# Kernel optimization log

Measured on AMD Instinct MI355X. Metric: run time of the kernel, lower is better.

The kernel has to match this reference:

```python
import jax, jax.numpy as jnp
import numpy as np

VOCAB = 50257
D_MEAN = 1024
D_MV = 1024
BATCH = 32
SEQ_LEN = 128


def setup_inputs() -> dict:
    key = jax.random.key(0)
    k_z, k_lab, k_w0, k_w1 = jax.random.split(key, 4)
    z = jax.random.normal(k_z, (BATCH, D_MEAN), dtype=jnp.float32)
    labels = jax.random.randint(k_lab, (BATCH, SEQ_LEN), 0, VOCAB, dtype=jnp.int64)
    # Linear weights stored as [in, out]; scaled like kaiming-uniform-ish init
    W0 = jax.random.normal(k_w0, (D_MEAN, D_MV), dtype=jnp.float32) * (1.0 / np.sqrt(D_MEAN))
    b0 = jnp.zeros((D_MV,), dtype=jnp.float32)
    W1 = jax.random.normal(k_w1, (D_MV, VOCAB), dtype=jnp.float32) * (1.0 / np.sqrt(D_MV))
    b1 = jnp.zeros((VOCAB,), dtype=jnp.float32)
    return {"z": z, "labels": labels, "W0": W0, "b0": b0, "W1": W1, "b1": b1}


def reference(z, labels, W0, b0, W1, b1):
    # bow_head: Linear -> Dropout(eval=identity) -> GELU -> Linear -> Dropout
    h = jax.nn.gelu(z @ W0 + b0, approximate=False)        # [B, d_mean_var]
    logits = h @ W1 + b1                                   # [B, vocab]
    # CrossEntropyLoss over logits expanded across seq_len == mean over
    # (B*seq_len) of NLL; log_softmax computed once per batch row and the
    # label gather reused across seq_len (same math, no expand materialized).
    logp = jax.nn.log_softmax(logits, axis=-1)             # [B, vocab]
    nll = -jnp.take_along_axis(logp, labels, axis=1)       # [B, seq_len]
    return jnp.mean(nll)
```

## Files before the change

### kernel.cpp

```cpp
#include <hip/hip_runtime.h>
#include <math.h>

#define VOCAB 50257
#define DMEAN 1024
#define DMV   1024
#define BATCH 32
#define SEQLEN 128
#define NS1 32
#define NS2 8
#define KC2 (DMV / NS2)
#define VP  50304
#define VPH (VP / 2)
#define CH3 2048
#define NB3 ((VP + CH3 - 1) / CH3)

static __device__ inline unsigned f2bf(float x) {
    unsigned u = __float_as_uint(x);
    return (u + 0x7fffu + ((u >> 16) & 1u)) >> 16;
}

__global__ __launch_bounds__(256) void k1_partial(const float* __restrict__ z,
                                                  const float* __restrict__ W0,
                                                  float* __restrict__ part) {
    int tx = threadIdx.x;
    int j  = blockIdx.x * 256 + tx;
    int k0 = blockIdx.y * (DMEAN / NS1);
    float acc[BATCH];
#pragma unroll
    for (int r = 0; r < BATCH; ++r) acc[r] = 0.f;
#pragma unroll 8
    for (int k = k0; k < k0 + (DMEAN / NS1); ++k) {
        float w = W0[k * DMV + j];
#pragma unroll
        for (int r = 0; r < BATCH; ++r)
            acc[r] = fmaf(z[r * DMEAN + k], w, acc[r]);
    }
#pragma unroll
    for (int r = 0; r < BATCH; ++r)
        part[(blockIdx.y * BATCH + r) * DMV + j] = acc[r];
}

__global__ __launch_bounds__(256) void k1_combine(const float* __restrict__ part,
                                                  const float* __restrict__ b0,
                                                  float* __restrict__ hT) {
    int t  = blockIdx.x * 256 + threadIdx.x;
    int e0 = t * 4;
    int r  = e0 >> 10;
    int j  = e0 & 1023;
    float4 s = *(const float4*)(b0 + j);
#pragma unroll
    for (int kb = 0; kb < NS1; ++kb) {
        float4 p = *(const float4*)(part + kb * BATCH * DMV + e0);
        s.x += p.x; s.y += p.y; s.z += p.z; s.w += p.w;
    }
    float v[4] = {s.x, s.y, s.z, s.w};
#pragma unroll
    for (int u = 0; u < 4; ++u) {
        float g = 0.5f * v[u] * (1.f + erff(v[u] * 0.70710678118654752f));
        hT[(j + u) * BATCH + r] = g;
    }
}

__global__ __launch_bounds__(256, 4) void k2_part(const float* __restrict__ hT,
                                                  const float* __restrict__ W1,
                                                  unsigned* __restrict__ part2) {
    int tx = threadIdx.x;
    int nb = blockIdx.x * 512 + tx * 2;
    int nn = min(nb, VOCAB - 2);
    int k0 = blockIdx.y * KC2;
    float accA[BATCH], accB[BATCH];
#pragma unroll
    for (int r = 0; r < BATCH; ++r) { accA[r] = 0.f; accB[r] = 0.f; }

    const float*  w  = W1 + (size_t)k0 * VOCAB + nn;
    const float4* hp = (const float4*)(hT + (size_t)k0 * BATCH);
#pragma unroll 2
    for (int k = 0; k < KC2; ++k) {
        float w0 = w[0];
        float w1 = w[1];
        w += VOCAB;
        float4 ha[4];
#pragma unroll
        for (int q = 0; q < 4; ++q) ha[q] = hp[q];
        const float* hva = (const float*)ha;
#pragma unroll
        for (int r = 0; r < 16; ++r) {
            accA[r] = fmaf(hva[r], w0, accA[r]);
            accB[r] = fmaf(hva[r], w1, accB[r]);
        }
        float4 hb[4];
#pragma unroll
        for (int q = 0; q < 4; ++q) hb[q] = hp[q + 4];
        const float* hvb = (const float*)hb;
#pragma unroll
        for (int r = 0; r < 16; ++r) {
            accA[r + 16] = fmaf(hvb[r], w0, accA[r + 16]);
            accB[r + 16] = fmaf(hvb[r], w1, accB[r + 16]);
        }
        hp += 8;
    }
    if (nb < VP) {
        unsigned* p = part2 + (size_t)blockIdx.y * BATCH * VPH + (nb >> 1);
#pragma unroll
        for (int r = 0; r < BATCH; ++r)
            p[(size_t)r * VPH] = f2bf(accA[r]) | (f2bf(accB[r]) << 16);
    }
}

__device__ inline float block_reduce_sum(float v, float* red) {
    int tx = threadIdx.x;
#pragma unroll
    for (int off = 32; off > 0; off >>= 1) v += __shfl_down(v, off, 64);
    if ((tx & 63) == 0) red[tx >> 6] = v;
    __syncthreads();
    float res = (red[0] + red[1]) + (red[2] + red[3]);
    __syncthreads();
    return res;
}

__global__ __launch_bounds__(256) void k3_stream(const unsigned* __restrict__ part2,
                                                 const float* __restrict__ b1,
                                                 const int* __restrict__ labels,
                                                 float* __restrict__ se_out,
                                                 float* __restrict__ g_out) {
    __shared__ float sval[CH3];
    __shared__ float red[4];
    int chunk = blockIdx.x, r = blockIdx.y, tx = threadIdx.x;
    int n0 = chunk * CH3 + tx * 8;

    float v[8];
#pragma unroll
    for (int u = 0; u < 8; ++u) v[u] = 0.f;
#pragma unroll
    for (int cs = 0; cs < NS2; ++cs) {
        const unsigned* base = part2 + ((size_t)cs * BATCH + r) * VPH + (n0 >> 1);
        uint4 pv = *(const uint4*)base;
        unsigned pw[4] = {pv.x, pv.y, pv.z, pv.w};
#pragma unroll
        for (int q = 0; q < 4; ++q) {
            v[2 * q]     += __uint_as_float(pw[q] << 16);
            v[2 * q + 1] += __uint_as_float(pw[q] & 0xffff0000u);
        }
    }

    float e = 0.f;
    if (n0 + 7 < VOCAB) {
        float4 ba = *(const float4*)(b1 + n0);
        float4 bb = *(const float4*)(b1 + n0 + 4);
        float bv[8] = {ba.x, ba.y, ba.z, ba.w, bb.x, bb.y, bb.z, bb.w};
#pragma unroll
        for (int u = 0; u < 8; ++u) {
            float lg = v[u] + bv[u];
            sval[tx * 8 + u] = lg;
            e += expf(lg);
        }
    } else {
#pragma unroll
        for (int u = 0; u < 8; ++u) {
            int n = n0 + u;
            float lg = (n < VOCAB) ? (v[u] + b1[n]) : 0.f;
            sval[tx * 8 + u] = lg;
            if (n < VOCAB) e += expf(lg);
        }
    }
    e = block_reduce_sum(e, red);
    if (tx == 0) se_out[r * NB3 + chunk] = e;

    float g = 0.f;
    if (tx < SEQLEN) {
        int lab = labels[r * SEQLEN + tx];
        unsigned d = (unsigned)(lab - chunk * CH3);
        if (d < (unsigned)CH3) g = sval[d];
    }
    g = block_reduce_sum(g, red);
    if (tx == 0) g_out[chunk * BATCH + r] = g;
}

__global__ __launch_bounds__(256) void k4_final(const float* __restrict__ se,
                                                const float* __restrict__ g_part,
                                                float* __restrict__ out) {
    __shared__ float red[4];
    __shared__ float lses[BATCH];
    int tx = threadIdx.x;
    int r = tx >> 3, l8 = tx & 7;
    float s = 0.f;
    for (int c = l8; c < NB3; c += 8) s += se[r * NB3 + c];
#pragma unroll
    for (int off = 4; off > 0; off >>= 1) s += __shfl_down(s, off, 8);
    if (l8 == 0) lses[r] = logf(s);

    float g = 0.f;
    for (int i = tx; i < NB3 * BATCH; i += 256) g += g_part[i];
    g = block_reduce_sum(g, red);

    if (tx == 0) {
        float L = 0.f;
#pragma unroll
        for (int r2 = 0; r2 < BATCH; ++r2) L += lses[r2];
        out[0] = ((float)SEQLEN * L - g) / (float)(BATCH * SEQLEN);
    }
}

extern "C" void kernel_launch(void* const* d_in, const int* in_sizes, int n_in,
                              void* d_out, int out_size, void* d_ws, size_t ws_size,
                              hipStream_t stream) {
    const float* z      = (const float*)d_in[0];
    const int*   labels = (const int*)  d_in[1];
    const float* W0     = (const float*)d_in[2];
    const float* b0     = (const float*)d_in[3];
    const float* W1     = (const float*)d_in[4];
    const float* b1     = (const float*)d_in[5];
    float* out = (float*)d_out;
    float* ws  = (float*)d_ws;

    float*    part1 = ws;
    float*    hT    = part1 + (size_t)NS1 * BATCH * DMV;
    unsigned* part2 = (unsigned*)(hT + (size_t)DMV * BATCH);
    float*    se    = (float*)(part2 + (size_t)NS2 * BATCH * VPH);
    float*    gpart = se + (size_t)BATCH * NB3;

    k1_partial<<<dim3(4, NS1), 256, 0, stream>>>(z, W0, part1);
    k1_combine<<<32, 256, 0, stream>>>(part1, b0, hT);
    k2_part<<<dim3((VOCAB + 511) / 512, NS2), 256, 0, stream>>>(hT, W1, part2);
    k3_stream<<<dim3(NB3, BATCH), 256, 0, stream>>>(part2, b1, labels, se, gpart);
    k4_final<<<1, 256, 0, stream>>>(se, gpart, out);
}
```

Measured before the change: 88.45 us.

## Use one column per thread in W1 GEMV with register-prefetched weight pipeline

The W1 projection kernel now assigns one vocab column per thread instead of two, which doubles the grid and halves the accumulator registers. It software-pipelines the strided W1 loads through an 8-deep register buffer so weight fetches overlap the FMA work. Each output pair is packed into bf16 via a lane shuffle and written by even lanes. The padded vocab is raised to a multiple of the chunk size so the streaming kernel's block count divides evenly. In exchange, the hT broadcast loads are now issued once per column rather than shared across two, and odd lanes sit idle during the stores.

```diff
diff --git a/kernel.cpp b/kernel.cpp
--- a/kernel.cpp
+++ b/kernel.cpp
@@ -9,10 +9,10 @@
 #define NS1 32
 #define NS2 8
 #define KC2 (DMV / NS2)
-#define VP  50304
+#define CH3 2048
+#define VP  51200
 #define VPH (VP / 2)
-#define CH3 2048
-#define NB3 ((VP + CH3 - 1) / CH3)
+#define NB3 (VP / CH3)
 
 static __device__ inline unsigned f2bf(float x) {
     unsigned u = __float_as_uint(x);
@@ -65,45 +65,59 @@
                                                   const float* __restrict__ W1,
                                                   unsigned* __restrict__ part2) {
     int tx = threadIdx.x;
-    int nb = blockIdx.x * 512 + tx * 2;
-    int nn = min(nb, VOCAB - 2);
+    int n  = blockIdx.x * 256 + tx;
+    int nn = min(n, VOCAB - 1);
     int k0 = blockIdx.y * KC2;
-    float accA[BATCH], accB[BATCH];
-#pragma unroll
-    for (int r = 0; r < BATCH; ++r) { accA[r] = 0.f; accB[r] = 0.f; }
-
-    const float*  w  = W1 + (size_t)k0 * VOCAB + nn;
+    float acc[BATCH];
+#pragma unroll
+    for (int r = 0; r < BATCH; ++r) acc[r] = 0.f;
+
+    const float*  wp = W1 + (size_t)k0 * VOCAB + nn;
     const float4* hp = (const float4*)(hT + (size_t)k0 * BATCH);
-#pragma unroll 2
-    for (int k = 0; k < KC2; ++k) {
-        float w0 = w[0];
-        float w1 = w[1];
-        w += VOCAB;
-        float4 ha[4];
-#pragma unroll
-        for (int q = 0; q < 4; ++q) ha[q] = hp[q];
-        const float* hva = (const float*)ha;
-#pragma unroll
-        for (int r = 0; r < 16; ++r) {
-            accA[r] = fmaf(hva[r], w0, accA[r]);
-            accB[r] = fmaf(hva[r], w1, accB[r]);
-        }
-        float4 hb[4];
-#pragma unroll
-        for (int q = 0; q < 4; ++q) hb[q] = hp[q + 4];
-        const float* hvb = (const float*)hb;
-#pragma unroll
-        for (int r = 0; r < 16; ++r) {
-            accA[r + 16] = fmaf(hvb[r], w0, accA[r + 16]);
-            accB[r + 16] = fmaf(hvb[r], w1, accB[r + 16]);
-        }
-        hp += 8;
-    }
-    if (nb < VP) {
-        unsigned* p = part2 + (size_t)blockIdx.y * BATCH * VPH + (nb >> 1);
+
+    float wbuf[8];
+#pragma unroll
+    for (int u = 0; u < 8; ++u) wbuf[u] = wp[(size_t)u * VOCAB];
+    const float* wnext = wp + (size_t)8 * VOCAB;
+
+    for (int kb = 0; kb < KC2 - 8; kb += 8) {
+#pragma unroll
+        for (int u = 0; u < 8; ++u) {
+            float wv = wbuf[u];
+            wbuf[u] = *wnext;
+            wnext  += VOCAB;
+            const float4* hk = hp + (kb + u) * 8;
+            float4 h4[8];
+#pragma unroll
+            for (int q = 0; q < 8; ++q) h4[q] = hk[q];
+            const float* hv = (const float*)h4;
+#pragma unroll
+            for (int r = 0; r < BATCH; ++r)
+                acc[r] = fmaf(hv[r], wv, acc[r]);
+        }
+    }
+#pragma unroll
+    for (int u = 0; u < 8; ++u) {
+        float wv = wbuf[u];
+        const float4* hk = hp + (KC2 - 8 + u) * 8;
+        float4 h4[8];
+#pragma unroll
+        for (int q = 0; q < 8; ++q) h4[q] = hk[q];
+        const float* hv = (const float*)h4;
 #pragma unroll
         for (int r = 0; r < BATCH; ++r)
-            p[(size_t)r * VPH] = f2bf(accA[r]) | (f2bf(accB[r]) << 16);
+            acc[r] = fmaf(hv[r], wv, acc[r]);
+    }
+
+    if (n < VP) {
+        unsigned* p = part2 + (size_t)blockIdx.y * BATCH * VPH + (n >> 1);
+        bool even = (tx & 1) == 0;
+#pragma unroll
+        for (int r = 0; r < BATCH; ++r) {
+            float other = __shfl_xor(acc[r], 1, 64);
+            unsigned pk = f2bf(acc[r]) | (f2bf(other) << 16);
+            if (even) p[(size_t)r * VPH] = pk;
+        }
     }
 }
 
@@ -221,7 +235,7 @@
 
     k1_partial<<<dim3(4, NS1), 256, 0, stream>>>(z, W0, part1);
     k1_combine<<<32, 256, 0, stream>>>(part1, b0, hT);
-    k2_part<<<dim3((VOCAB + 511) / 512, NS2), 256, 0, stream>>>(hT, W1, part2);
+    k2_part<<<dim3((VOCAB + 255) / 256, NS2), 256, 0, stream>>>(hT, W1, part2);
     k3_stream<<<dim3(NB3, BATCH), 256, 0, stream>>>(part2, b1, labels, se, gpart);
     k4_final<<<1, 256, 0, stream>>>(se, gpart, out);
 }
```

After: 119.6 us. +35.2%, slower.
